# Optimization experiments

Measured on AMD Instinct MI355X. Metric: run time of the kernel, lower is better.

The kernel has to match this reference:

```python
import jax, jax.numpy as jnp
import numpy as np

N, E = 50000, 800000
DIN, DH, DOUT = 128, 128, 64


def setup_inputs() -> dict:
    key = jax.random.key(0)
    k = jax.random.split(key, 6)
    node_features = jax.random.normal(k[0], (N, DIN), dtype=jnp.float32)
    edge_src = jax.random.randint(k[1], (E,), 0, N)
    edge_dst = jax.random.randint(k[2], (E,), 0, N)
    # Glorot-ish init for the two GCNConv weight matrices, zero bias (PyG default bias=True)
    W1 = jax.random.normal(k[3], (DIN, DH), dtype=jnp.float32) * (1.0 / np.sqrt(DIN))
    b1 = jnp.zeros((DH,), dtype=jnp.float32)
    W2 = jax.random.normal(k[4], (DH, DOUT), dtype=jnp.float32) * (1.0 / np.sqrt(DH))
    b2 = jnp.zeros((DOUT,), dtype=jnp.float32)
    return {"node_features": node_features, "edge_src": edge_src, "edge_dst": edge_dst,
            "W1": W1, "b1": b1, "W2": W2, "b2": b2}


def gcn_conv(x, W, b, src, dst, n):
    """PyG GCNConv: add self-loops, symmetric D^-1/2 (A+I) D^-1/2 normalization."""
    xw = x @ W  # [n, d_out]
    loops = jnp.arange(n, dtype=src.dtype)
    s = jnp.concatenate([src, loops])  # edges + self-loops
    d = jnp.concatenate([dst, loops])
    deg = jax.ops.segment_sum(jnp.ones_like(d, dtype=xw.dtype), d, num_segments=n)
    dinv = jnp.where(deg > 0, jax.lax.rsqrt(deg), 0.0)
    norm = dinv[s] * dinv[d]  # [E + n]
    msg = xw[s] * norm[:, None]  # gather + scale (memory-bound)
    out = jax.ops.segment_sum(msg, d, num_segments=n)  # scatter-add
    return out + b


def reference(node_features, edge_src, edge_dst, W1, b1, W2, b2):
    n = node_features.shape[0]
    h = gcn_conv(node_features, W1, b1, edge_src, edge_dst, n)
    h = jax.nn.relu(h)  # dropout omitted (inference / eval mode)
    h = gcn_conv(h, W2, b2, edge_src, edge_dst, n)
    # EdgePredictor: per-edge dot product of endpoint representations
    score = jnp.sum(h[edge_src] * h[edge_dst], axis=-1)  # [E]
    return score
```

## Files before the change

kernel.cpp:

```cpp
#include <hip/hip_runtime.h>
#include <hip/hip_bf16.h>
#include <type_traits>


#define DIN 128
#define DH  128
#define DOUT 64
#define CAP 4608

typedef __attribute__((ext_vector_type(8))) short short8;
typedef __attribute__((ext_vector_type(4))) float floatx4;

__device__ inline float2 bf2_to_f2(unsigned u) {
    union { unsigned i; float f; } a, b;
    a.i = u << 16;
    b.i = u & 0xffff0000u;
    return make_float2(a.f, b.f);
}
__device__ inline float bf_to_f(unsigned short u) {
    union { unsigned i; float f; } a;
    a.i = ((unsigned)u) << 16;
    return a.f;
}
__device__ inline unsigned short f_to_bf(float f) {
    union { float f; unsigned i; } v; v.f = f;
    unsigned r = v.i + 0x7fffu + ((v.i >> 16) & 1u);
    return (unsigned short)(r >> 16);
}

__global__ __launch_bounds__(256) void place_kernel(const int* __restrict__ src,
                                                    const int* __restrict__ dst,
                                                    int* __restrict__ cursor,
                                                    uint2* __restrict__ tmp, int E) {
    __shared__ int hist[256];
    __shared__ int cur[256];
    int t = threadIdx.x;
    hist[t] = 0;
    __syncthreads();
    int base = blockIdx.x * 4096 + t;
    int d[16];
#pragma unroll
    for (int it = 0; it < 16; ++it) {
        int e = base + it * 256;
        d[it] = (e < E) ? dst[e] : -1;
        if (d[it] >= 0) atomicAdd(&hist[d[it] >> 8], 1);
    }
    __syncthreads();
    if (hist[t]) cur[t] = atomicAdd(&cursor[t], hist[t]);
    __syncthreads();
#pragma unroll
    for (int it = 0; it < 16; ++it) {
        int e = base + it * 256;
        if (d[it] >= 0) {
            int bkt = d[it] >> 8;
            int r = atomicAdd(&cur[bkt], 1);
            if (r < CAP)
                tmp[(size_t)bkt * CAP + r] =
                    make_uint2((unsigned)src[e] | ((unsigned)(d[it] & 255) << 16),
                               (unsigned)e);
        }
    }
}

__global__ __launch_bounds__(256) void bucket_csr_kernel(const uint2* __restrict__ tmp,
                                                         const int* __restrict__ cursor,
                                                         int* __restrict__ row_beg,
                                                         int* __restrict__ row_end,
                                                         float* __restrict__ dinv,
                                                         int* __restrict__ col,
                                                         int* __restrict__ eidx, int N) {
    __shared__ int hist[256], cur[256], pfx[256];
    __shared__ unsigned ebuf[CAP];
    __shared__ unsigned ibuf[CAP];
    __shared__ unsigned ssrc[CAP];
    __shared__ unsigned sidx[CAP];
    int b = blockIdx.x, t = threadIdx.x;
    int size = cursor[b];
    if (size > CAP) size = CAP;
    size_t rbase = (size_t)b * CAP;
    hist[t] = 0;
    __syncthreads();
    for (int i = t; i < size; i += 256) {
        uint2 e = tmp[rbase + i];
        ebuf[i] = e.x;
        ibuf[i] = e.y;
        atomicAdd(&hist[e.x >> 16], 1);
    }
    __syncthreads();
    int v = hist[t];
    pfx[t] = v;
    __syncthreads();
    for (int off = 1; off < 256; off <<= 1) {
        int u = (t >= off) ? pfx[t - off] : 0;
        __syncthreads();
        pfx[t] += u;
        __syncthreads();
    }
    int ex = pfx[t] - v;
    cur[t] = ex;
    int node = b * 256 + t;
    if (node < N) {
        row_beg[node] = (int)rbase + ex;
        row_end[node] = (int)rbase + ex + v;
        dinv[node] = rsqrtf((float)(v + 1));
    }
    __syncthreads();
    for (int i = t; i < size; i += 256) {
        int r = atomicAdd(&cur[ebuf[i] >> 16], 1);
        ssrc[r] = ebuf[i] & 0xffffu;
        sidx[r] = ibuf[i];
    }
    __syncthreads();
    for (int i = t; i < size; i += 256) {
        col[rbase + i]  = (int)ssrc[i];
        eidx[rbase + i] = (int)sidx[i];
    }
}

template <int COLS, typename XT>
__global__ __launch_bounds__(256) void mfma_gemm_kernel(const XT* __restrict__ X,
                                                        const float* __restrict__ W,
                                                        const float* __restrict__ dinv,
                                                        unsigned short* __restrict__ Y,
                                                        int nrows) {
    constexpr int KP = 136;
    __shared__ unsigned short Xs[128 * KP];
    __shared__ unsigned short Wt[COLS * KP];
    int tid = threadIdx.x;
    int row0 = blockIdx.x * 128;

    if constexpr (std::is_same_v<XT, float>) {
#pragma unroll
        for (int it = 0; it < 16; ++it) {
            int idx = it * 256 + tid;
            int r = idx >> 5;
            int c4 = (idx & 31) * 4;
            int gr = row0 + r; if (gr >= nrows) gr = nrows - 1;
            float4 v = *(const float4*)(X + (size_t)gr * 128 + c4);
            ushort4 p;
            p.x = f_to_bf(v.x); p.y = f_to_bf(v.y);
            p.z = f_to_bf(v.z); p.w = f_to_bf(v.w);
            *(ushort4*)&Xs[r * KP + c4] = p;
        }
    } else {
#pragma unroll
        for (int it = 0; it < 8; ++it) {
            int idx = it * 256 + tid;
            int r = idx >> 4;
            int c8 = (idx & 15) * 8;
            int gr = row0 + r; if (gr >= nrows) gr = nrows - 1;
            uint4 v = *(const uint4*)(X + (size_t)gr * 128 + c8);
            *(uint4*)&Xs[r * KP + c8] = v;
        }
    }
#pragma unroll
    for (int it = 0; it < COLS / 8; ++it) {
        int idx = it * 256 + tid;
        int n = idx >> 5;
        int k4 = (idx & 31) * 4;
        ushort4 p;
        p.x = f_to_bf(W[(size_t)(k4 + 0) * COLS + n]);
        p.y = f_to_bf(W[(size_t)(k4 + 1) * COLS + n]);
        p.z = f_to_bf(W[(size_t)(k4 + 2) * COLS + n]);
        p.w = f_to_bf(W[(size_t)(k4 + 3) * COLS + n]);
        *(ushort4*)&Wt[n * KP + k4] = p;
    }
    __syncthreads();

    constexpr int CT = COLS / 16;
    int wv = tid >> 6, lane = tid & 63;
    int lr = lane & 15;
    int lk = (lane >> 4) * 8;
    int rw = wv * 32;

    floatx4 acc[2][CT];
#pragma unroll
    for (int rt = 0; rt < 2; ++rt)
#pragma unroll
        for (int ct = 0; ct < CT; ++ct) acc[rt][ct] = (floatx4){0.f, 0.f, 0.f, 0.f};

#pragma unroll
    for (int kk = 0; kk < 128; kk += 32) {
        short8 a[2], b[CT];
#pragma unroll
        for (int rt = 0; rt < 2; ++rt)
            a[rt] = *(const short8*)&Xs[(rw + rt * 16 + lr) * KP + kk + lk];
#pragma unroll
        for (int ct = 0; ct < CT; ++ct)
            b[ct] = *(const short8*)&Wt[(ct * 16 + lr) * KP + kk + lk];
#pragma unroll
        for (int rt = 0; rt < 2; ++rt)
#pragma unroll
            for (int ct = 0; ct < CT; ++ct)
                acc[rt][ct] = __builtin_amdgcn_mfma_f32_16x16x32_bf16(
                    a[rt], b[ct], acc[rt][ct], 0, 0, 0);
    }

#pragma unroll
    for (int rt = 0; rt < 2; ++rt) {
#pragma unroll
        for (int i = 0; i < 4; ++i) {
            int grow = row0 + rw + rt * 16 + (lane >> 4) * 4 + i;
            if (grow >= nrows) continue;
            float dv = dinv[grow];
#pragma unroll
            for (int ct = 0; ct < CT; ++ct)
                Y[(size_t)grow * COLS + ct * 16 + lr] =
                    f_to_bf(acc[rt][ct][i] * dv);
        }
    }
}

template <int D, bool RELU>
__global__ __launch_bounds__(256) void agg_kernel(const unsigned short* __restrict__ y,
                                                  const int* __restrict__ row_beg,
                                                  const int* __restrict__ row_end,
                                                  const int* __restrict__ col,
                                                  const float* __restrict__ dinv,
                                                  const float* __restrict__ bias,
                                                  unsigned short* __restrict__ out, int n) {
    constexpr int V = D / 64;
    int w = (blockIdx.x * 256 + threadIdx.x) >> 6;
    int lane = threadIdx.x & 63;
    if (w >= n) return;
    float acc[V];
    if constexpr (V == 2) {
        float2 t = bf2_to_f2(*(const unsigned*)(y + (size_t)w * D + lane * 2));
        acc[0] = t.x; acc[1] = t.y;
    } else {
        acc[0] = bf_to_f(y[(size_t)w * D + lane]);
    }
    int beg = row_beg[w], end = row_end[w];
    int i = beg;
    for (; i + 8 <= end; i += 8) {
        int s[8];
#pragma unroll
        for (int u = 0; u < 8; ++u) s[u] = col[i + u];
        if constexpr (V == 2) {
            unsigned tv[8];
#pragma unroll
            for (int u = 0; u < 8; ++u)
                tv[u] = *(const unsigned*)(y + (size_t)s[u] * D + lane * 2);
#pragma unroll
            for (int u = 0; u < 8; ++u) {
                float2 f = bf2_to_f2(tv[u]);
                acc[0] += f.x; acc[1] += f.y;
            }
        } else {
            unsigned short tv[8];
#pragma unroll
            for (int u = 0; u < 8; ++u) tv[u] = y[(size_t)s[u] * D + lane];
#pragma unroll
            for (int u = 0; u < 8; ++u) acc[0] += bf_to_f(tv[u]);
        }
    }
    for (; i < end; ++i) {
        int s = col[i];
        if constexpr (V == 2) {
            float2 f = bf2_to_f2(*(const unsigned*)(y + (size_t)s * D + lane * 2));
            acc[0] += f.x; acc[1] += f.y;
        } else {
            acc[0] += bf_to_f(y[(size_t)s * D + lane]);
        }
    }
    float dv = dinv[w];
    if constexpr (V == 2) {
        float r0 = fmaf(dv, acc[0], bias[lane * 2]);
        float r1 = fmaf(dv, acc[1], bias[lane * 2 + 1]);
        if (RELU) { r0 = fmaxf(r0, 0.f); r1 = fmaxf(r1, 0.f); }
        unsigned pk = (unsigned)f_to_bf(r0) | ((unsigned)f_to_bf(r1) << 16);
        *(unsigned*)(out + (size_t)w * D + lane * 2) = pk;
    } else {
        float r = fmaf(dv, acc[0], bias[lane]);
        if (RELU) r = fmaxf(r, 0.f);
        out[(size_t)w * D + lane] = f_to_bf(r);
    }
}

__global__ __launch_bounds__(256) void score_csr_kernel(const unsigned short* __restrict__ h2,
                                                        const int* __restrict__ row_beg,
                                                        const int* __restrict__ row_end,
                                                        const int* __restrict__ col,
                                                        const int* __restrict__ eidx,
                                                        float* __restrict__ out, int n) {
    int w = (blockIdx.x * 256 + threadIdx.x) >> 6;
    int lane = threadIdx.x & 63;
    if (w >= n) return;
    int q = lane & 7;
    uint4 hd = *(const uint4*)(h2 + (size_t)w * 64 + q * 8);
    float d0[8];
    { float2 f;
      f = bf2_to_f2(hd.x); d0[0] = f.x; d0[1] = f.y;
      f = bf2_to_f2(hd.y); d0[2] = f.x; d0[3] = f.y;
      f = bf2_to_f2(hd.z); d0[4] = f.x; d0[5] = f.y;
      f = bf2_to_f2(hd.w); d0[6] = f.x; d0[7] = f.y; }
    int beg = row_beg[w], end = row_end[w];
    int g = lane >> 3;
    for (int i = beg; i < end; i += 8) {
        int ei = i + g;
        bool ok = ei < end;
        int s = ok ? col[ei] : 0;
        uint4 hs = *(const uint4*)(h2 + (size_t)s * 64 + q * 8);
        float v = 0.f;
        float2 f;
        f = bf2_to_f2(hs.x); v = fmaf(d0[0], f.x, v); v = fmaf(d0[1], f.y, v);
        f = bf2_to_f2(hs.y); v = fmaf(d0[2], f.x, v); v = fmaf(d0[3], f.y, v);
        f = bf2_to_f2(hs.z); v = fmaf(d0[4], f.x, v); v = fmaf(d0[5], f.y, v);
        f = bf2_to_f2(hs.w); v = fmaf(d0[6], f.x, v); v = fmaf(d0[7], f.y, v);
        v += __shfl_xor(v, 4);
        v += __shfl_xor(v, 2);
        v += __shfl_xor(v, 1);
        if (ok && q == 0) out[eidx[ei]] = v;
    }
}

extern "C" void kernel_launch(void* const* d_in, const int* in_sizes, int n_in,
                              void* d_out, int out_size, void* d_ws, size_t ws_size,
                              hipStream_t stream) {
    const float* X   = (const float*)d_in[0];
    const int*   src = (const int*)d_in[1];
    const int*   dst = (const int*)d_in[2];
    const float* W1  = (const float*)d_in[3];
    const float* b1  = (const float*)d_in[4];
    const float* W2  = (const float*)d_in[5];
    const float* b2  = (const float*)d_in[6];
    float* score = (float*)d_out;

    const int N = in_sizes[0] / DIN;
    const int E = in_sizes[1];
    const int nbuck = (N + 255) / 256;
    const int EB = (E + 4095) / 4096;

    auto align = [](size_t x) { return (x + 255) & ~(size_t)255; };
    char* p = (char*)d_ws;
    int*   cursor  = (int*)p;               p += align(256 * 4);
    int*   row_beg = (int*)p;               p += align((size_t)N * 4);
    int*   row_end = (int*)p;               p += align((size_t)N * 4);
    float* dinv    = (float*)p;             p += align((size_t)N * 4);
    int*   col     = (int*)p;               p += align((size_t)nbuck * CAP * 4);
    int*   eidx    = (int*)p;               p += align((size_t)nbuck * CAP * 4);
    uint2* tmp     = (uint2*)p;             p += align((size_t)nbuck * CAP * 8);
    unsigned short* y1 = (unsigned short*)p; p += align((size_t)N * DH * 2);
    unsigned short* h1 = (unsigned short*)p; p += align((size_t)N * DH * 2);
    unsigned short* y2 = y1;
    unsigned short* h2 = y1 + (size_t)N * DOUT;

    hipMemsetAsync(cursor, 0, 256 * 4, stream);

    place_kernel<<<EB, 256, 0, stream>>>(src, dst, cursor, tmp, E);
    bucket_csr_kernel<<<nbuck, 256, 0, stream>>>(tmp, cursor, row_beg, row_end,
                                                 dinv, col, eidx, N);

    int gemm_blocks = (N + 127) / 128;
    mfma_gemm_kernel<DH, float><<<gemm_blocks, 256, 0, stream>>>(X, W1, dinv, y1, N);

    int agg_blocks = (N + 3) / 4;
    agg_kernel<DH, true><<<agg_blocks, 256, 0, stream>>>(y1, row_beg, row_end,
                                                         col, dinv, b1, h1, N);

    mfma_gemm_kernel<DOUT, unsigned short><<<gemm_blocks, 256, 0, stream>>>(h1, W2, dinv, y2, N);
    agg_kernel<DOUT, false><<<agg_blocks, 256, 0, stream>>>(y2, row_beg, row_end,
                                                            col, dinv, b2, h2, N);

    score_csr_kernel<<<agg_blocks, 256, 0, stream>>>(h2, row_beg, row_end,
                                                     col, eidx, score, N);
}
```

Measured before the change: 247.2 us.

## Fuse edge placement with GEMM1 and layer-1 aggregation with GEMM2

The edge bucketing pass and the first X·W1 GEMM now run in one launch as disjoint block ranges, so GEMM1 can no longer use dinv and the source-side normalisation moves into the aggregation as a per-neighbour dinv gather. Layer-1 aggregation now also computes the second projection per node using wave shuffles and W2 held in shared memory, which removes the h1 intermediate and one GEMM launch. The cost is an extra dinv gather per edge, a scalar FMA GEMM instead of MFMA for layer 2, and 32KB of shared-memory W2 loaded by every aggregation block.

```diff
diff --git a/kernel.cpp b/kernel.cpp
--- a/kernel.cpp
+++ b/kernel.cpp
@@ -1,6 +1,5 @@
 #include <hip/hip_runtime.h>
 #include <hip/hip_bf16.h>
-#include <type_traits>
 
 
 #define DIN 128
@@ -28,36 +27,113 @@
     return (unsigned short)(r >> 16);
 }
 
-__global__ __launch_bounds__(256) void place_kernel(const int* __restrict__ src,
-                                                    const int* __restrict__ dst,
-                                                    int* __restrict__ cursor,
-                                                    uint2* __restrict__ tmp, int E) {
-    __shared__ int hist[256];
-    __shared__ int cur[256];
-    int t = threadIdx.x;
-    hist[t] = 0;
-    __syncthreads();
-    int base = blockIdx.x * 4096 + t;
-    int d[16];
+__global__ __launch_bounds__(256) void place_gemm1_kernel(
+    const int* __restrict__ src, const int* __restrict__ dst,
+    int* __restrict__ cursor, uint2* __restrict__ tmp, int E, int EB,
+    const float* __restrict__ X, const float* __restrict__ W1,
+    unsigned short* __restrict__ Y, int nrows) {
+    __shared__ __align__(16) char smem[69632];
+    int bid = blockIdx.x, t = threadIdx.x;
+
+    if (bid < EB) {
+        int* hist = (int*)smem;
+        int* cur  = hist + 256;
+        hist[t] = 0;
+        __syncthreads();
+        int base = bid * 4096 + t;
+        int d[16];
+#pragma unroll
+        for (int it = 0; it < 16; ++it) {
+            int e = base + it * 256;
+            d[it] = (e < E) ? dst[e] : -1;
+            if (d[it] >= 0) atomicAdd(&hist[d[it] >> 8], 1);
+        }
+        __syncthreads();
+        if (hist[t]) cur[t] = atomicAdd(&cursor[t], hist[t]);
+        __syncthreads();
+#pragma unroll
+        for (int it = 0; it < 16; ++it) {
+            int e = base + it * 256;
+            if (d[it] >= 0) {
+                int bkt = d[it] >> 8;
+                int r = atomicAdd(&cur[bkt], 1);
+                if (r < CAP)
+                    tmp[(size_t)bkt * CAP + r] =
+                        make_uint2((unsigned)src[e] |
+                                   ((unsigned)(d[it] & 255) << 16),
+                                   (unsigned)e);
+            }
+        }
+        return;
+    }
+
+    constexpr int KP = 136;
+    unsigned short* Xs = (unsigned short*)smem;
+    unsigned short* Wt = Xs + 128 * KP;
+    int row0 = (bid - EB) * 128;
+
 #pragma unroll
     for (int it = 0; it < 16; ++it) {
-        int e = base + it * 256;
-        d[it] = (e < E) ? dst[e] : -1;
-        if (d[it] >= 0) atomicAdd(&hist[d[it] >> 8], 1);
-    }
-    __syncthreads();
-    if (hist[t]) cur[t] = atomicAdd(&cursor[t], hist[t]);
-    __syncthreads();
+        int idx = it * 256 + t;
+        int r = idx >> 5;
+        int c4 = (idx & 31) * 4;
+        int gr = row0 + r; if (gr >= nrows) gr = nrows - 1;
+        float4 v = *(const float4*)(X + (size_t)gr * 128 + c4);
+        ushort4 p;
+        p.x = f_to_bf(v.x); p.y = f_to_bf(v.y);
+        p.z = f_to_bf(v.z); p.w = f_to_bf(v.w);
+        *(ushort4*)&Xs[r * KP + c4] = p;
+    }
 #pragma unroll
     for (int it = 0; it < 16; ++it) {
-        int e = base + it * 256;
-        if (d[it] >= 0) {
-            int bkt = d[it] >> 8;
-            int r = atomicAdd(&cur[bkt], 1);
-            if (r < CAP)
-                tmp[(size_t)bkt * CAP + r] =
-                    make_uint2((unsigned)src[e] | ((unsigned)(d[it] & 255) << 16),
-                               (unsigned)e);
+        int idx = it * 256 + t;
+        int n = idx >> 5;
+        int k4 = (idx & 31) * 4;
+        ushort4 p;
+        p.x = f_to_bf(W1[(size_t)(k4 + 0) * 128 + n]);
+        p.y = f_to_bf(W1[(size_t)(k4 + 1) * 128 + n]);
+        p.z = f_to_bf(W1[(size_t)(k4 + 2) * 128 + n]);
+        p.w = f_to_bf(W1[(size_t)(k4 + 3) * 128 + n]);
+        *(ushort4*)&Wt[n * KP + k4] = p;
+    }
+    __syncthreads();
+
+    int wv = t >> 6, lane = t & 63;
+    int lr = lane & 15;
+    int lk = (lane >> 4) * 8;
+    int rw = wv * 32;
+
+    floatx4 acc[2][8];
+#pragma unroll
+    for (int rt = 0; rt < 2; ++rt)
+#pragma unroll
+        for (int ct = 0; ct < 8; ++ct) acc[rt][ct] = (floatx4){0.f, 0.f, 0.f, 0.f};
+
+#pragma unroll
+    for (int kk = 0; kk < 128; kk += 32) {
+        short8 a[2], b[8];
+#pragma unroll
+        for (int rt = 0; rt < 2; ++rt)
+            a[rt] = *(const short8*)&Xs[(rw + rt * 16 + lr) * KP + kk + lk];
+#pragma unroll
+        for (int ct = 0; ct < 8; ++ct)
+            b[ct] = *(const short8*)&Wt[(ct * 16 + lr) * KP + kk + lk];
+#pragma unroll
+        for (int rt = 0; rt < 2; ++rt)
+#pragma unroll
+            for (int ct = 0; ct < 8; ++ct)
+                acc[rt][ct] = __builtin_amdgcn_mfma_f32_16x16x32_bf16(
+                    a[rt], b[ct], acc[rt][ct], 0, 0, 0);
+    }
+#pragma unroll
+    for (int rt = 0; rt < 2; ++rt) {
+#pragma unroll
+        for (int i = 0; i < 4; ++i) {
+            int grow = row0 + rw + rt * 16 + (lane >> 4) * 4 + i;
+            if (grow >= nrows) continue;
+#pragma unroll
+            for (int ct = 0; ct < 8; ++ct)
+                Y[(size_t)grow * 128 + ct * 16 + lr] = f_to_bf(acc[rt][ct][i]);
         }
     }
 }
@@ -117,118 +193,28 @@
     }
 }
 
-template <int COLS, typename XT>
-__global__ __launch_bounds__(256) void mfma_gemm_kernel(const XT* __restrict__ X,
-                                                        const float* __restrict__ W,
-                                                        const float* __restrict__ dinv,
-                                                        unsigned short* __restrict__ Y,
-                                                        int nrows) {
-    constexpr int KP = 136;
-    __shared__ unsigned short Xs[128 * KP];
-    __shared__ unsigned short Wt[COLS * KP];
+__global__ __launch_bounds__(256) void agg1_gemm2_kernel(
+    const unsigned short* __restrict__ y1, const int* __restrict__ row_beg,
+    const int* __restrict__ row_end, const int* __restrict__ col,
+    const float* __restrict__ dinv, const float* __restrict__ b1,
+    const float* __restrict__ W2, unsigned short* __restrict__ y2, int n) {
+    __shared__ float W2s[128 * 64];
     int tid = threadIdx.x;
-    int row0 = blockIdx.x * 128;
-
-    if constexpr (std::is_same_v<XT, float>) {
-#pragma unroll
-        for (int it = 0; it < 16; ++it) {
-            int idx = it * 256 + tid;
-            int r = idx >> 5;
-            int c4 = (idx & 31) * 4;
-            int gr = row0 + r; if (gr >= nrows) gr = nrows - 1;
-            float4 v = *(const float4*)(X + (size_t)gr * 128 + c4);
-            ushort4 p;
-            p.x = f_to_bf(v.x); p.y = f_to_bf(v.y);
-            p.z = f_to_bf(v.z); p.w = f_to_bf(v.w);
-            *(ushort4*)&Xs[r * KP + c4] = p;
-        }
-    } else {
-#pragma unroll
-        for (int it = 0; it < 8; ++it) {
-            int idx = it * 256 + tid;
-            int r = idx >> 4;
-            int c8 = (idx & 15) * 8;
-            int gr = row0 + r; if (gr >= nrows) gr = nrows - 1;
-            uint4 v = *(const uint4*)(X + (size_t)gr * 128 + c8);
-            *(uint4*)&Xs[r * KP + c8] = v;
-        }
-    }
-#pragma unroll
-    for (int it = 0; it < COLS / 8; ++it) {
+#pragma unroll
+    for (int it = 0; it < 8; ++it) {
         int idx = it * 256 + tid;
-        int n = idx >> 5;
-        int k4 = (idx & 31) * 4;
-        ushort4 p;
-        p.x = f_to_bf(W[(size_t)(k4 + 0) * COLS + n]);
-        p.y = f_to_bf(W[(size_t)(k4 + 1) * COLS + n]);
-        p.z = f_to_bf(W[(size_t)(k4 + 2) * COLS + n]);
-        p.w = f_to_bf(W[(size_t)(k4 + 3) * COLS + n]);
-        *(ushort4*)&Wt[n * KP + k4] = p;
-    }
-    __syncthreads();
-
-    constexpr int CT = COLS / 16;
-    int wv = tid >> 6, lane = tid & 63;
-    int lr = lane & 15;
-    int lk = (lane >> 4) * 8;
-    int rw = wv * 32;
-
-    floatx4 acc[2][CT];
-#pragma unroll
-    for (int rt = 0; rt < 2; ++rt)
-#pragma unroll
-        for (int ct = 0; ct < CT; ++ct) acc[rt][ct] = (floatx4){0.f, 0.f, 0.f, 0.f};
-
-#pragma unroll
-    for (int kk = 0; kk < 128; kk += 32) {
-        short8 a[2], b[CT];
-#pragma unroll
-        for (int rt = 0; rt < 2; ++rt)
-            a[rt] = *(const short8*)&Xs[(rw + rt * 16 + lr) * KP + kk + lk];
-#pragma unroll
-        for (int ct = 0; ct < CT; ++ct)
-            b[ct] = *(const short8*)&Wt[(ct * 16 + lr) * KP + kk + lk];
-#pragma unroll
-        for (int rt = 0; rt < 2; ++rt)
-#pragma unroll
-            for (int ct = 0; ct < CT; ++ct)
-                acc[rt][ct] = __builtin_amdgcn_mfma_f32_16x16x32_bf16(
-                    a[rt], b[ct], acc[rt][ct], 0, 0, 0);
-    }
-
-#pragma unroll
-    for (int rt = 0; rt < 2; ++rt) {
-#pragma unroll
-        for (int i = 0; i < 4; ++i) {
-            int grow = row0 + rw + rt * 16 + (lane >> 4) * 4 + i;
-            if (grow >= nrows) continue;
-            float dv = dinv[grow];
-#pragma unroll
-            for (int ct = 0; ct < CT; ++ct)
-                Y[(size_t)grow * COLS + ct * 16 + lr] =
-                    f_to_bf(acc[rt][ct][i] * dv);
-        }
-    }
-}
-
-template <int D, bool RELU>
-__global__ __launch_bounds__(256) void agg_kernel(const unsigned short* __restrict__ y,
-                                                  const int* __restrict__ row_beg,
-                                                  const int* __restrict__ row_end,
-                                                  const int* __restrict__ col,
-                                                  const float* __restrict__ dinv,
-                                                  const float* __restrict__ bias,
-                                                  unsigned short* __restrict__ out, int n) {
-    constexpr int V = D / 64;
-    int w = (blockIdx.x * 256 + threadIdx.x) >> 6;
-    int lane = threadIdx.x & 63;
+        *(float4*)&W2s[idx * 4] = *(const float4*)(W2 + (size_t)idx * 4);
+    }
+    __syncthreads();
+
+    int w = (blockIdx.x * 256 + tid) >> 6;
+    int lane = tid & 63;
     if (w >= n) return;
-    float acc[V];
-    if constexpr (V == 2) {
-        float2 t = bf2_to_f2(*(const unsigned*)(y + (size_t)w * D + lane * 2));
-        acc[0] = t.x; acc[1] = t.y;
-    } else {
-        acc[0] = bf_to_f(y[(size_t)w * D + lane]);
+    float dw = dinv[w];
+    float acc0, acc1;
+    {
+        float2 t2 = bf2_to_f2(*(const unsigned*)(y1 + (size_t)w * 128 + lane * 2));
+        acc0 = dw * t2.x; acc1 = dw * t2.y;
     }
     int beg = row_beg[w], end = row_end[w];
     int i = beg;
@@ -236,45 +222,67 @@
         int s[8];
 #pragma unroll
         for (int u = 0; u < 8; ++u) s[u] = col[i + u];
-        if constexpr (V == 2) {
-            unsigned tv[8];
-#pragma unroll
-            for (int u = 0; u < 8; ++u)
-                tv[u] = *(const unsigned*)(y + (size_t)s[u] * D + lane * 2);
-#pragma unroll
-            for (int u = 0; u < 8; ++u) {
-                float2 f = bf2_to_f2(tv[u]);
-                acc[0] += f.x; acc[1] += f.y;
-            }
-        } else {
-            unsigned short tv[8];
-#pragma unroll
-            for (int u = 0; u < 8; ++u) tv[u] = y[(size_t)s[u] * D + lane];
-#pragma unroll
-            for (int u = 0; u < 8; ++u) acc[0] += bf_to_f(tv[u]);
+        float dv[8];
+#pragma unroll
+        for (int u = 0; u < 8; ++u) dv[u] = dinv[s[u]];
+        unsigned tv[8];
+#pragma unroll
+        for (int u = 0; u < 8; ++u)
+            tv[u] = *(const unsigned*)(y1 + (size_t)s[u] * 128 + lane * 2);
+#pragma unroll
+        for (int u = 0; u < 8; ++u) {
+            float2 f = bf2_to_f2(tv[u]);
+            acc0 = fmaf(dv[u], f.x, acc0);
+            acc1 = fmaf(dv[u], f.y, acc1);
         }
     }
     for (; i < end; ++i) {
         int s = col[i];
-        if constexpr (V == 2) {
-            float2 f = bf2_to_f2(*(const unsigned*)(y + (size_t)s * D + lane * 2));
-            acc[0] += f.x; acc[1] += f.y;
-        } else {
-            acc[0] += bf_to_f(y[(size_t)s * D + lane]);
-        }
-    }
-    float dv = dinv[w];
-    if constexpr (V == 2) {
-        float r0 = fmaf(dv, acc[0], bias[lane * 2]);
-        float r1 = fmaf(dv, acc[1], bias[lane * 2 + 1]);
-        if (RELU) { r0 = fmaxf(r0, 0.f); r1 = fmaxf(r1, 0.f); }
-        unsigned pk = (unsigned)f_to_bf(r0) | ((unsigned)f_to_bf(r1) << 16);
-        *(unsigned*)(out + (size_t)w * D + lane * 2) = pk;
-    } else {
-        float r = fmaf(dv, acc[0], bias[lane]);
-        if (RELU) r = fmaxf(r, 0.f);
-        out[(size_t)w * D + lane] = f_to_bf(r);
-    }
+        float dv = dinv[s];
+        float2 f = bf2_to_f2(*(const unsigned*)(y1 + (size_t)s * 128 + lane * 2));
+        acc0 = fmaf(dv, f.x, acc0);
+        acc1 = fmaf(dv, f.y, acc1);
+    }
+    float h0 = fmaxf(fmaf(dw, acc0, b1[lane * 2]), 0.f);
+    float h1 = fmaxf(fmaf(dw, acc1, b1[lane * 2 + 1]), 0.f);
+
+    float acc2 = 0.f;
+#pragma unroll 8
+    for (int j = 0; j < 64; ++j) {
+        float a = __shfl(h0, j);
+        float b = __shfl(h1, j);
+        acc2 = fmaf(a, W2s[(2 * j) * 64 + lane], acc2);
+        acc2 = fmaf(b, W2s[(2 * j + 1) * 64 + lane], acc2);
+    }
+    y2[(size_t)w * 64 + lane] = f_to_bf(dw * acc2);
+}
+
+__global__ __launch_bounds__(256) void agg2_kernel(const unsigned short* __restrict__ y,
+                                                   const int* __restrict__ row_beg,
+                                                   const int* __restrict__ row_end,
+                                                   const int* __restrict__ col,
+                                                   const float* __restrict__ dinv,
+                                                   const float* __restrict__ bias,
+                                                   unsigned short* __restrict__ out, int n) {
+    int w = (blockIdx.x * 256 + threadIdx.x) >> 6;
+    int lane = threadIdx.x & 63;
+    if (w >= n) return;
+    float acc = bf_to_f(y[(size_t)w * 64 + lane]);
+    int beg = row_beg[w], end = row_end[w];
+    int i = beg;
+    for (; i + 8 <= end; i += 8) {
+        int s[8];
+#pragma unroll
+        for (int u = 0; u < 8; ++u) s[u] = col[i + u];
+        unsigned short tv[8];
+#pragma unroll
+        for (int u = 0; u < 8; ++u) tv[u] = y[(size_t)s[u] * 64 + lane];
+#pragma unroll
+        for (int u = 0; u < 8; ++u) acc += bf_to_f(tv[u]);
+    }
+    for (; i < end; ++i) acc += bf_to_f(y[(size_t)col[i] * 64 + lane]);
+    float r = fmaf(dinv[w], acc, bias[lane]);
+    out[(size_t)w * 64 + lane] = f_to_bf(r);
 }
 
 __global__ __launch_bounds__(256) void score_csr_kernel(const unsigned short* __restrict__ h2,
@@ -330,6 +338,7 @@
     const int E = in_sizes[1];
     const int nbuck = (N + 255) / 256;
     const int EB = (E + 4095) / 4096;
+    const int GB = (N + 127) / 128;
 
     auto align = [](size_t x) { return (x + 255) & ~(size_t)255; };
     char* p = (char*)d_ws;
@@ -341,27 +350,21 @@
     int*   eidx    = (int*)p;               p += align((size_t)nbuck * CAP * 4);
     uint2* tmp     = (uint2*)p;             p += align((size_t)nbuck * CAP * 8);
     unsigned short* y1 = (unsigned short*)p; p += align((size_t)N * DH * 2);
-    unsigned short* h1 = (unsigned short*)p; p += align((size_t)N * DH * 2);
-    unsigned short* y2 = y1;
-    unsigned short* h2 = y1 + (size_t)N * DOUT;
+    unsigned short* y2 = (unsigned short*)p; p += align((size_t)N * DOUT * 2);
+    unsigned short* h2 = y1;
 
     hipMemsetAsync(cursor, 0, 256 * 4, stream);
 
-    place_kernel<<<EB, 256, 0, stream>>>(src, dst, cursor, tmp, E);
+    place_gemm1_kernel<<<EB + GB, 256, 0, stream>>>(src, dst, cursor, tmp, E, EB,
+                                                    X, W1, y1, N);
     bucket_csr_kernel<<<nbuck, 256, 0, stream>>>(tmp, cursor, row_beg, row_end,
                                                  dinv, col, eidx, N);
 
-    int gemm_blocks = (N + 127) / 128;
-    mfma_gemm_kernel<DH, float><<<gemm_blocks, 256, 0, stream>>>(X, W1, dinv, y1, N);
-
     int agg_blocks = (N + 3) / 4;
-    agg_kernel<DH, true><<<agg_blocks, 256, 0, stream>>>(y1, row_beg, row_end,
-                                                         col, dinv, b1, h1, N);
-
-    mfma_gemm_kernel<DOUT, unsigned short><<<gemm_blocks, 256, 0, stream>>>(h1, W2, dinv, y2, N);
-    agg_kernel<DOUT, false><<<agg_blocks, 256, 0, stream>>>(y2, row_beg, row_end,
-                                                            col, dinv, b2, h2, N);
-
+    agg1_gemm2_kernel<<<agg_blocks, 256, 0, stream>>>(y1, row_beg, row_end, col,
+                                                      dinv, b1, W2, y2, N);
+    agg2_kernel<<<agg_blocks, 256, 0, stream>>>(y2, row_beg, row_end, col,
+                                                dinv, b2, h2, N);
     score_csr_kernel<<<agg_blocks, 256, 0, stream>>>(h2, row_beg, row_end,
                                                      col, eidx, score, N);
 }
```

Result: slower. 305.4 us (+23.6%).
